# Kernel optimization log

Measured on AMD Instinct MI355X. Metric: run time of the kernel, lower is better.

Reference implementation:

```python
import jax, jax.numpy as jnp
import numpy as np

N = 16384       # pedestrian_num
D_IN = 2        # input_size
H = 64          # hidden_size


def setup_inputs() -> dict:
    key = jax.random.key(0)
    ks = jax.random.split(key, 4)
    data = jax.random.normal(ks[0], (N, D_IN), dtype=jnp.float32)
    # Linear weights stored as [in, out]; scaled like torch default init (~1/sqrt(in)).
    W1 = jax.random.normal(ks[1], (D_IN, 32), dtype=jnp.float32) / np.sqrt(D_IN)
    b1 = jnp.zeros((32,), dtype=jnp.float32)
    W2 = jax.random.normal(ks[2], (32, 64), dtype=jnp.float32) / np.sqrt(32)
    b2 = jnp.zeros((64,), dtype=jnp.float32)
    W3 = jax.random.normal(ks[3], (64, H), dtype=jnp.float32) / np.sqrt(64)
    b3 = jnp.zeros((H,), dtype=jnp.float32)
    return {"data": data, "W1": W1, "b1": b1, "W2": W2, "b2": b2, "W3": W3, "b3": b3}


def reference(data, W1, b1, W2, b2, W3, b3):
    # Per-pedestrian MLP (batched over all N pedestrians at once).
    h = jax.nn.relu(data @ W1 + b1)          # [N, 32]
    h = jax.nn.relu(h @ W2 + b2)             # [N, 64]
    h = h @ W3 + b3                          # [N, H]
    # Spatial affinity: the original fills the lower triangle with <h_i, h_j>
    # and its softmax reads entry [max(i,j), min(i,j)], i.e. the full
    # symmetric Gram matrix G = h @ h.T.
    G = jnp.einsum("nd,md->nm", h, h)        # [N, N], symmetric
    # Row-wise softmax over the symmetric affinity matrix.
    return jax.nn.softmax(G, axis=-1)
```

## Files before the change

kernel.cpp:

```cpp
#include <hip/hip_runtime.h>

#define N     16384
#define DH    64
#define TILE  128
#define NT    (N / TILE)
#define S2    133

typedef __attribute__((ext_vector_type(8))) short  short8;
typedef __attribute__((ext_vector_type(4))) float  f32x4;

__device__ __forceinline__ ushort bf_hi(float x) {
    unsigned u = __float_as_uint(x);
    unsigned r = u + 0x7FFFu + ((u >> 16) & 1u);
    return (ushort)(r >> 16);
}
__device__ __forceinline__ float bf_val(ushort h) {
    return __uint_as_float(((unsigned)h) << 16);
}

__device__ __forceinline__ short8 ldfrag(const ushort* __restrict__ p, int row, int koff) {
    return *(const short8*)(p + (size_t)row * DH + koff);
}

__global__ __launch_bounds__(128) void mlp_kernel(
    const float* __restrict__ data,
    const float* __restrict__ W1, const float* __restrict__ b1,
    const float* __restrict__ W2, const float* __restrict__ b2,
    const float* __restrict__ W3, const float* __restrict__ b3,
    ushort* __restrict__ hHi, ushort* __restrict__ hLo)
{
    __shared__ float sW1[64], sb1[32], sW2[32 * 64], sb2[64], sW3[64 * 64], sb3[64];
    const int tid = threadIdx.x;
    if (tid < 64) sW1[tid] = W1[tid];
    if (tid < 32) sb1[tid] = b1[tid];
    if (tid < 64) sb2[tid] = b2[tid];
    if (tid < 64) sb3[tid] = b3[tid];
    for (int t = tid; t < 32 * 64; t += 128) sW2[t] = W2[t];
    for (int t = tid; t < 64 * 64; t += 128) sW3[t] = W3[t];
    __syncthreads();

    const int i = blockIdx.x * 128 + tid;
    const float x0 = data[2 * i + 0];
    const float x1 = data[2 * i + 1];

    float h1[32];
#pragma unroll
    for (int o = 0; o < 32; ++o)
        h1[o] = fmaxf(0.f, fmaf(x0, sW1[o], fmaf(x1, sW1[32 + o], sb1[o])));

    float h2[64];
#pragma unroll
    for (int o = 0; o < 64; ++o) {
        float a = sb2[o];
#pragma unroll
        for (int k = 0; k < 32; ++k) a = fmaf(h1[k], sW2[k * 64 + o], a);
        h2[o] = fmaxf(0.f, a);
    }

    ushort hs[64], ls[64];
#pragma unroll
    for (int o = 0; o < 64; ++o) {
        float a = sb3[o];
#pragma unroll
        for (int k = 0; k < 64; ++k) a = fmaf(h2[k], sW3[k * 64 + o], a);
        const ushort hb = bf_hi(a);
        hs[o] = hb;
        ls[o] = bf_hi(a - bf_val(hb));
    }
#pragma unroll
    for (int q = 0; q < 8; ++q) {
        short8 vh, vl;
#pragma unroll
        for (int t = 0; t < 8; ++t) { vh[t] = (short)hs[q * 8 + t]; vl[t] = (short)ls[q * 8 + t]; }
        *(short8*)(hHi + (size_t)i * DH + q * 8) = vh;
        *(short8*)(hLo + (size_t)i * DH + q * 8) = vl;
    }
}

__device__ __forceinline__ void stage_B(
    const ushort* __restrict__ hHi, const ushort* __restrict__ hLo,
    int brow0, int tid, ushort* __restrict__ sB)
{
    const int arr = tid >> 7;
    const int r   = tid & 127;
    const ushort* __restrict__ src = (arr ? hLo : hHi) + (size_t)(brow0 + r) * DH;
    ushort* __restrict__ dst = sB + arr * (TILE * DH) + r * 64;
    const int sw = (r & 7);
#pragma unroll
    for (int q = 0; q < 8; ++q) {
        const short8 v = *(const short8*)(src + q * 8);
        *(short8*)(dst + 8 * (q ^ sw)) = v;
    }
}

__device__ __forceinline__ short8 ldB(const ushort* __restrict__ sB,
                                      int arr, int row, int ks, int kb)
{
    return *(const short8*)(sB + arr * (TILE * DH) + row * 64 + 8 * (((ks << 2) + kb) ^ (row & 7)));
}

__device__ __forceinline__ void gram_tile(
    const ushort* __restrict__ hHi, const ushort* __restrict__ hLo,
    const ushort* __restrict__ sB,
    int bi, int wave, int r16, int kb, f32x4 acc[2][8])
{
#pragma unroll
    for (int rb = 0; rb < 2; ++rb)
#pragma unroll
        for (int cb = 0; cb < 8; ++cb) acc[rb][cb] = (f32x4){0.f, 0.f, 0.f, 0.f};

    const int arow = bi * TILE + wave * 16 + r16;
    short8 Ah[2][2], Al[2][2];
#pragma unroll
    for (int rb = 0; rb < 2; ++rb)
#pragma unroll
        for (int ks = 0; ks < 2; ++ks) {
            Ah[rb][ks] = ldfrag(hHi, arow + rb * 64, ks * 32 + kb * 8);
            Al[rb][ks] = ldfrag(hLo, arow + rb * 64, ks * 32 + kb * 8);
        }

#pragma unroll
    for (int cb = 0; cb < 8; ++cb) {
        const int brow = cb * 16 + r16;
        short8 Bh[2], Bl[2];
#pragma unroll
        for (int ks = 0; ks < 2; ++ks) {
            Bh[ks] = ldB(sB, 0, brow, ks, kb);
            Bl[ks] = ldB(sB, 1, brow, ks, kb);
        }
#pragma unroll
        for (int rb = 0; rb < 2; ++rb)
#pragma unroll
            for (int ks = 0; ks < 2; ++ks) {
                acc[rb][cb] = __builtin_amdgcn_mfma_f32_16x16x32_bf16(Ah[rb][ks], Bh[ks], acc[rb][cb], 0, 0, 0);
                acc[rb][cb] = __builtin_amdgcn_mfma_f32_16x16x32_bf16(Ah[rb][ks], Bl[ks], acc[rb][cb], 0, 0, 0);
                acc[rb][cb] = __builtin_amdgcn_mfma_f32_16x16x32_bf16(Al[rb][ks], Bh[ks], acc[rb][cb], 0, 0, 0);
            }
    }
}

__device__ __forceinline__ int tile_row(int wave, int kb, int rb, int reg) {
    return rb * 64 + wave * 16 + kb * 4 + reg;
}

#define SMEM_BYTES 34048

__global__ __launch_bounds__(256) void pass1_mfma(
    const ushort* __restrict__ hHi, const ushort* __restrict__ hLo,
    float* __restrict__ part_m, float* __restrict__ part_l)
{
    const int p = blockIdx.x;
    const int xcd = p & 7, s = p >> 3;
    const int q = s / 129, r = s % 129;
    const int P = xcd * 8 + q;
    int bi, bj;
    if (r <= P) { bi = r;         bj = P;       }
    else        { bi = r - P - 1; bj = 127 - P; }

    __shared__ __attribute__((aligned(16))) char smem[SMEM_BYTES];
    ushort* sB = (ushort*)smem;
    float*  jm = (float*)smem;
    float*  jl = jm + 512;

    const int tid = threadIdx.x;
    const int wave = tid >> 6, lane = tid & 63;
    const int r16 = lane & 15, kb = lane >> 4;

    stage_B(hHi, hLo, bj * TILE, tid, sB);
    __syncthreads();

    f32x4 acc[2][8];
    gram_tile(hHi, hLo, sB, bi, wave, r16, kb, acc);

#pragma unroll
    for (int rb = 0; rb < 2; ++rb) {
#pragma unroll
        for (int reg = 0; reg < 4; ++reg) {
            float m = acc[rb][0][reg];
#pragma unroll
            for (int cb = 1; cb < 8; ++cb) m = fmaxf(m, acc[rb][cb][reg]);
            m = fmaxf(m, __shfl_xor(m, 1));
            m = fmaxf(m, __shfl_xor(m, 2));
            m = fmaxf(m, __shfl_xor(m, 4));
            m = fmaxf(m, __shfl_xor(m, 8));
            float sum = 0.f;
#pragma unroll
            for (int cb = 0; cb < 8; ++cb) sum += __expf(acc[rb][cb][reg] - m);
            sum += __shfl_xor(sum, 1);
            sum += __shfl_xor(sum, 2);
            sum += __shfl_xor(sum, 4);
            sum += __shfl_xor(sum, 8);
            if (r16 == 0) {
                const int grow = bi * TILE + tile_row(wave, kb, rb, reg);
                part_m[(size_t)bj * N + grow] = m;
                part_l[(size_t)bj * N + grow] = sum;
            }
        }
    }

    if (bi != bj) {
        __syncthreads();
#pragma unroll
        for (int cb = 0; cb < 8; ++cb) {
            float m = acc[0][cb][0];
#pragma unroll
            for (int rb = 0; rb < 2; ++rb)
#pragma unroll
                for (int reg = 0; reg < 4; ++reg) m = fmaxf(m, acc[rb][cb][reg]);
            m = fmaxf(m, __shfl_xor(m, 16));
            m = fmaxf(m, __shfl_xor(m, 32));
            float sum = 0.f;
#pragma unroll
            for (int rb = 0; rb < 2; ++rb)
#pragma unroll
                for (int reg = 0; reg < 4; ++reg) sum += __expf(acc[rb][cb][reg] - m);
            sum += __shfl_xor(sum, 16);
            sum += __shfl_xor(sum, 32);
            if (kb == 0) { jm[wave * 128 + cb * 16 + r16] = m; jl[wave * 128 + cb * 16 + r16] = sum; }
        }
        __syncthreads();
        if (tid < 128) {
            float M = jm[tid];
#pragma unroll
            for (int w = 1; w < 4; ++w) M = fmaxf(M, jm[w * 128 + tid]);
            float L = 0.f;
#pragma unroll
            for (int w = 0; w < 4; ++w) L += jl[w * 128 + tid] * __expf(jm[w * 128 + tid] - M);
            part_m[(size_t)bi * N + bj * TILE + tid] = M;
            part_l[(size_t)bi * N + bj * TILE + tid] = L;
        }
    }
}

__global__ __launch_bounds__(256) void merge_kernel(
    const float* __restrict__ part_m, const float* __restrict__ part_l,
    float* __restrict__ mrow, float* __restrict__ rrow)
{
    const int i = blockIdx.x * 256 + threadIdx.x;
    float M = -3.0e38f;
    for (int o = 0; o < NT; ++o) M = fmaxf(M, part_m[(size_t)o * N + i]);
    float L = 0.f;
    for (int o = 0; o < NT; ++o)
        L = fmaf(part_l[(size_t)o * N + i], __expf(part_m[(size_t)o * N + i] - M), L);
    mrow[i] = M;
    rrow[i] = 1.0f / L;
}

__global__ __launch_bounds__(256) void pass2_mfma(
    const ushort* __restrict__ hHi, const ushort* __restrict__ hLo,
    const float* __restrict__ mrow, const float* __restrict__ rrow,
    float* __restrict__ out)
{
    const int p = blockIdx.x;
    const int xcd = p & 7, slot = p >> 3;
    const int bj = xcd * 16 + (slot & 15);
    const int bi = slot >> 4;

    const int tid = threadIdx.x;
    const int wave = tid >> 6, lane = tid & 63;
    const int r16 = lane & 15, kb = lane >> 4;

    __shared__ __attribute__((aligned(16))) char smem[SMEM_BYTES];
    ushort* sB   = (ushort*)smem;
    float*  ldsP = (float*)smem;

    stage_B(hHi, hLo, bj * TILE, tid, sB);
    __syncthreads();

    f32x4 acc[2][8];
    gram_tile(hHi, hLo, sB, bi, wave, r16, kb, acc);
    __syncthreads();

#pragma unroll
    for (int hh = 0; hh < 2; ++hh) {
#pragma unroll
        for (int reg = 0; reg < 4; ++reg) {
            const int rl   = wave * 16 + kb * 4 + reg;
            const int grow = bi * TILE + hh * 64 + rl;
            const float m  = mrow[grow];
            const float rr = rrow[grow];
#pragma unroll
            for (int cb = 0; cb < 8; ++cb)
                ldsP[rl * S2 + cb * 16 + r16] = __expf(acc[hh][cb][reg] - m) * rr;
        }
        __syncthreads();
#pragma unroll
        for (int qq = 0; qq < 8; ++qq) {
            const int f4 = tid + 256 * qq;
            const int rl = f4 >> 5, c4 = f4 & 31;
            const f32x4 v = *(const f32x4*)&ldsP[rl * S2 + c4 * 4];
            f32x4* dst = (f32x4*)(out + (size_t)(bi * TILE + hh * 64 + rl) * N + bj * TILE + c4 * 4);
            __builtin_nontemporal_store(v, dst);
        }
        __syncthreads();
    }
}

extern "C" void kernel_launch(void* const* d_in, const int* in_sizes, int n_in,
                              void* d_out, int out_size, void* d_ws, size_t ws_size,
                              hipStream_t stream)
{
    const float* data = (const float*)d_in[0];
    const float* W1   = (const float*)d_in[1];
    const float* b1   = (const float*)d_in[2];
    const float* W2   = (const float*)d_in[3];
    const float* b2   = (const float*)d_in[4];
    const float* W3   = (const float*)d_in[5];
    const float* b3   = (const float*)d_in[6];
    float* out = (float*)d_out;

    float* part_m = (float*)d_ws;
    float* part_l = part_m + (size_t)NT * N;
    float* mrow   = part_l + (size_t)NT * N;
    float* rrow   = mrow + N;
    ushort* hHi   = (ushort*)(rrow + N);
    ushort* hLo   = hHi + (size_t)N * DH;

    mlp_kernel<<<N / 128, 128, 0, stream>>>(data, W1, b1, W2, b2, W3, b3, hHi, hLo);
    pass1_mfma<<<NT * (NT + 1) / 2, 256, 0, stream>>>(hHi, hLo, part_m, part_l);
    merge_kernel<<<N / 256, 256, 0, stream>>>(part_m, part_l, mrow, rrow);
    pass2_mfma<<<NT * NT, 256, 0, stream>>>(hHi, hLo, mrow, rrow, out);
}
```

Measured before the change: 370.7 us.

## Exploit Gram symmetry in pass2 to compute only upper-triangle tiles

Pass2 now launches only the triangular set of tile pairs and, for each computed Gram tile, writes both the tile for (bi,bj) and its transpose for (bj,bi). Each is normalised with its own row's max and reciprocal sum. This roughly halves the MFMA work and B staging in pass2, which matters little if the kernel is bound by writing the output. The transposed write path does strided LDS reads and stores in 16-byte chunks per column, which may be less coalesced. Diagonal tiles are written twice with identical values.

```diff
diff --git a/kernel.cpp b/kernel.cpp
--- a/kernel.cpp
+++ b/kernel.cpp
@@ -143,19 +143,22 @@
     return rb * 64 + wave * 16 + kb * 4 + reg;
 }
 
+__device__ __forceinline__ void tri_decode(int p, int& bi, int& bj) {
+    const int xcd = p & 7, s = p >> 3;
+    const int q = s / 129, r = s % 129;
+    const int P = xcd * 8 + q;
+    if (r <= P) { bi = r;         bj = P;       }
+    else        { bi = r - P - 1; bj = 127 - P; }
+}
+
 #define SMEM_BYTES 34048
 
 __global__ __launch_bounds__(256) void pass1_mfma(
     const ushort* __restrict__ hHi, const ushort* __restrict__ hLo,
     float* __restrict__ part_m, float* __restrict__ part_l)
 {
-    const int p = blockIdx.x;
-    const int xcd = p & 7, s = p >> 3;
-    const int q = s / 129, r = s % 129;
-    const int P = xcd * 8 + q;
     int bi, bj;
-    if (r <= P) { bi = r;         bj = P;       }
-    else        { bi = r - P - 1; bj = 127 - P; }
+    tri_decode(blockIdx.x, bi, bj);
 
     __shared__ __attribute__((aligned(16))) char smem[SMEM_BYTES];
     ushort* sB = (ushort*)smem;
@@ -251,10 +254,8 @@
     const float* __restrict__ mrow, const float* __restrict__ rrow,
     float* __restrict__ out)
 {
-    const int p = blockIdx.x;
-    const int xcd = p & 7, slot = p >> 3;
-    const int bj = xcd * 16 + (slot & 15);
-    const int bi = slot >> 4;
+    int bi, bj;
+    tri_decode(blockIdx.x, bi, bj);
 
     const int tid = threadIdx.x;
     const int wave = tid >> 6, lane = tid & 63;
@@ -262,7 +263,7 @@
 
     __shared__ __attribute__((aligned(16))) char smem[SMEM_BYTES];
     ushort* sB   = (ushort*)smem;
-    float*  ldsP = (float*)smem;
+    float*  ldsG = (float*)smem;
 
     stage_B(hHi, hLo, bj * TILE, tid, sB);
     __syncthreads();
@@ -275,21 +276,43 @@
     for (int hh = 0; hh < 2; ++hh) {
 #pragma unroll
         for (int reg = 0; reg < 4; ++reg) {
-            const int rl   = wave * 16 + kb * 4 + reg;
+            const int rl = wave * 16 + kb * 4 + reg;
+#pragma unroll
+            for (int cb = 0; cb < 8; ++cb)
+                ldsG[rl * S2 + cb * 16 + r16] = acc[hh][cb][reg];
+        }
+        __syncthreads();
+
+#pragma unroll
+        for (int qq = 0; qq < 8; ++qq) {
+            const int f4 = tid + 256 * qq;
+            const int rl = f4 >> 5, c4 = f4 & 31;
             const int grow = bi * TILE + hh * 64 + rl;
             const float m  = mrow[grow];
             const float rr = rrow[grow];
-#pragma unroll
-            for (int cb = 0; cb < 8; ++cb)
-                ldsP[rl * S2 + cb * 16 + r16] = __expf(acc[hh][cb][reg] - m) * rr;
-        }
-        __syncthreads();
+            const f32x4 g = *(const f32x4*)&ldsG[rl * S2 + c4 * 4];
+            f32x4 v;
+            v.x = __expf(g.x - m) * rr;
+            v.y = __expf(g.y - m) * rr;
+            v.z = __expf(g.z - m) * rr;
+            v.w = __expf(g.w - m) * rr;
+            f32x4* dst = (f32x4*)(out + (size_t)grow * N + bj * TILE + c4 * 4);
+            __builtin_nontemporal_store(v, dst);
+        }
+
 #pragma unroll
         for (int qq = 0; qq < 8; ++qq) {
             const int f4 = tid + 256 * qq;
-            const int rl = f4 >> 5, c4 = f4 & 31;
-            const f32x4 v = *(const f32x4*)&ldsP[rl * S2 + c4 * 4];
-            f32x4* dst = (f32x4*)(out + (size_t)(bi * TILE + hh * 64 + rl) * N + bj * TILE + c4 * 4);
+            const int c = f4 >> 4, rr4 = f4 & 15;
+            const int gcol = bj * TILE + c;
+            const float m  = mrow[gcol];
+            const float rc = rrow[gcol];
+            f32x4 v;
+            v.x = __expf(ldsG[(rr4 * 4 + 0) * S2 + c] - m) * rc;
+            v.y = __expf(ldsG[(rr4 * 4 + 1) * S2 + c] - m) * rc;
+            v.z = __expf(ldsG[(rr4 * 4 + 2) * S2 + c] - m) * rc;
+            v.w = __expf(ldsG[(rr4 * 4 + 3) * S2 + c] - m) * rc;
+            f32x4* dst = (f32x4*)(out + (size_t)gcol * N + bi * TILE + hh * 64 + rr4 * 4);
             __builtin_nontemporal_store(v, dst);
         }
         __syncthreads();
@@ -319,5 +342,5 @@
     mlp_kernel<<<N / 128, 128, 0, stream>>>(data, W1, b1, W2, b2, W3, b3, hHi, hLo);
     pass1_mfma<<<NT * (NT + 1) / 2, 256, 0, stream>>>(hHi, hLo, part_m, part_l);
     merge_kernel<<<N / 256, 256, 0, stream>>>(part_m, part_l, mrow, rrow);
-    pass2_mfma<<<NT * NT, 256, 0, stream>>>(hHi, hLo, mrow, rrow, out);
-}
+    pass2_mfma<<<NT * (NT + 1) / 2, 256, 0, stream>>>(hHi, hLo, mrow, rrow, out);
+}
```

New measurement: 397.1 us. 1.07x slower.
